# Optimization experiments

Measured on AMD Instinct MI355X. Metric: run time of the kernel, lower is better.

## Reference

```python
import jax, jax.numpy as jnp
import numpy as np

H = 128        # hidden_dim
NP = 512       # program nodes
NV = 50000     # voxel nodes
E = 800000     # cross edges (16 per voxel)
TAU = 1.0
SLOPE = 0.01   # LeakyReLU default negative slope


def setup_inputs() -> dict:
    key = jax.random.key(0)
    ks = jax.random.split(key, 12)
    s = 1.0 / np.sqrt(H)
    x = jax.random.normal(ks[0], (NP, H), dtype=jnp.float32)
    v = jax.random.normal(ks[1], (NV, H), dtype=jnp.float32)
    row0 = jax.random.randint(ks[2], (E,), 0, NP, dtype=jnp.int32)
    row1 = (jnp.arange(E, dtype=jnp.int32) % NV)  # every voxel gets E/NV edges
    cross_edge_index = jnp.stack([row0, row1])    # [2, E]
    W_program = jax.random.normal(ks[3], (H, H), dtype=jnp.float32) * s
    b_program = jnp.zeros((H,), dtype=jnp.float32)
    W_voxel = jax.random.normal(ks[4], (H, H), dtype=jnp.float32) * s
    b_voxel = jnp.zeros((H,), dtype=jnp.float32)
    W_m1 = jax.random.normal(ks[5], (H, H), dtype=jnp.float32) * s
    b_m1 = jnp.zeros((H,), dtype=jnp.float32)
    W_m2 = jax.random.normal(ks[6], (H, 1), dtype=jnp.float32) * s
    b_m2 = jnp.zeros((1,), dtype=jnp.float32)
    theta = jax.random.normal(ks[7], (H, 1), dtype=jnp.float32) * s  # xavier-like
    u = jax.random.uniform(ks[8], (E,), dtype=jnp.float32)
    gumbel_u = jnp.clip(u, 1e-7, 1.0 - 1e-7)  # avoid log(0)
    return {"x": x, "v": v, "cross_edge_index": cross_edge_index,
            "W_program": W_program, "b_program": b_program,
            "W_voxel": W_voxel, "b_voxel": b_voxel,
            "W_m1": W_m1, "b_m1": b_m1, "W_m2": W_m2, "b_m2": b_m2,
            "theta": theta, "gumbel_u": gumbel_u}


def reference(x, v, cross_edge_index, W_program, b_program, W_voxel, b_voxel,
              W_m1, b_m1, W_m2, b_m2, theta, gumbel_u):
    src = cross_edge_index[0]
    dst = cross_edge_index[1]
    x_sel = x[src]                      # [E, H] gather
    v_sel = v[dst]                      # [E, H] gather
    # mask = sigmoid(MLP(v)) : Linear -> LeakyReLU -> Linear(H,1)
    a = v @ W_m1 + b_m1
    a = jnp.where(a >= 0, a, SLOPE * a)
    mask = jax.nn.sigmoid(a @ W_m2 + b_m2)                  # [NV, 1]
    # attention logits: theta^T * tanh(Wp x_sel + Wv v_sel), summed over H
    t = jnp.tanh(x_sel @ W_program + b_program + v_sel @ W_voxel + b_voxel)
    e = jnp.sum(t * theta[:, 0], axis=-1)                   # [E]
    # Gumbel softmax: global softmax over all edges (dim=0 in torch on 1-D e)
    g = -jnp.log(-jnp.log(gumbel_u))
    y = jax.nn.softmax((e + g) / TAU)                       # [E]
    # per-voxel hard argmax (scatter_max), straight-through estimator
    seg_max = jax.ops.segment_max(y, dst, num_segments=NV)  # [NV]
    is_max = y == seg_max[dst]
    cand = jnp.where(is_max, jnp.arange(E), E)
    argmax = jax.ops.segment_min(cand, dst, num_segments=NV)  # [NV], first max per voxel
    y_hard_1 = jnp.zeros(E + 1, y.dtype).at[argmax].set(1.0)[:E]  # overflow slot for empty segments
    y_hard = jax.lax.stop_gradient(y_hard_1 - y) + y
    # scatter-sum of soft-attended program features back to voxels
    summed = jax.ops.segment_sum(x_sel * y[:, None], dst, num_segments=NV)  # [NV, H]
    v_out = v + mask * summed
    return (v_out, mask, y[:, None], y_hard[:, None])
```

## Files before the change

### kernel.cpp

```cpp
#include <hip/hip_runtime.h>

#define H     128
#define NP    512
#define NVOX  50000
#define NEDGE 800000
#define EPV   16
#define SLOPE 0.01f
#define GR    32
#define NBLK  1563
#define STRH  136
#define VSTR  132
#define C1    2.8853900817779268f
#define LOG2E 1.4426950408889634f
#define ABLK  3125

#define EXP2(x) __builtin_amdgcn_exp2f(x)
#define LOG2(x) __builtin_amdgcn_logf(x)
#define RCP(x)  __builtin_amdgcn_rcpf(x)

typedef _Float16 h16;
typedef __attribute__((ext_vector_type(4))) _Float16 h16x4;
typedef __attribute__((ext_vector_type(8))) _Float16 h16x8;
typedef __attribute__((ext_vector_type(4))) float    f32x4;

__global__ __launch_bounds__(256) void k_pre(const float* __restrict__ x,
                                             const float* __restrict__ Wp,
                                             const float* __restrict__ bp,
                                             const float* __restrict__ Wv,
                                             const float* __restrict__ Wm1,
                                             float* __restrict__ xpout,
                                             h16* __restrict__ WvThi,
                                             h16* __restrict__ WvTlo,
                                             h16* __restrict__ Wm1T) {
    __shared__ float part[H];
    int bid = blockIdx.x;
    int tid = threadIdx.x;
    if (bid < NP) {
        int row = bid;
        int col = tid & 127;
        int kh  = tid >> 7;
        int kbase = kh * 64;
        const float* xr = x + (size_t)row * H;
        float acc = 0.f;
#pragma unroll 8
        for (int k = 0; k < 64; ++k)
            acc = fmaf(xr[kbase + k], Wp[(size_t)(kbase + k) * H + col], acc);
        if (kh == 1) part[col] = acc;
        __syncthreads();
        if (kh == 0) xpout[(size_t)row * H + col] = (acc + part[col] + bp[col]) * C1;
    } else {
        int idx = (bid - NP) * 256 + tid;
        if (idx < 16384) {
            int k = idx >> 7, n = idx & 127;
            float w = Wv[idx];
            h16 hi = (h16)w;
            WvThi[n * H + k] = hi;
            WvTlo[n * H + k] = (h16)(w - (float)hi);
        } else {
            int j = idx - 16384;
            int k = j >> 7, n = j & 127;
            Wm1T[n * H + k] = (h16)Wm1[j];
        }
    }
}

__global__ __launch_bounds__(256, 4) void k_mainX(
    const float* __restrict__ v,   const float* __restrict__ x,
    const float* __restrict__ bv,  const float* __restrict__ bm1,
    const float* __restrict__ Wm2, const float* __restrict__ bm2,
    const h16* __restrict__ WvThi, const h16* __restrict__ WvTlo,
    const h16* __restrict__ Wm1T,
    const float* __restrict__ xp,  const int* __restrict__ cei,
    const float* __restrict__ theta, const float* __restrict__ gum,
    float* __restrict__ mask_out, float* __restrict__ pout,
    float* __restrict__ sump,     float* __restrict__ partial)
{
    __shared__ __align__(16) char ldsbuf[2 * GR * STRH * 2];
    h16*   vh = (h16*)ldsbuf;
    h16*   vl = vh + GR * STRH;
    float* vt = (float*)ldsbuf;
    __shared__ float ptile[EPV * GR];
    __shared__ int   ceit[EPV * GR];
    __shared__ float gumt[EPV * GR];
    __shared__ int   amtile[GR];
    __shared__ float pmbuf[4][GR];
    __shared__ float psums[4];

    int tid  = threadIdx.x;
    int base = blockIdx.x * GR;

#pragma unroll
    for (int i = 0; i < 4; ++i) {
        int f  = i * 256 + tid;
        int r  = f >> 5, c4 = f & 31;
        int gr = base + r; if (gr >= NVOX) gr = NVOX - 1;
        float4 val = *(const float4*)&v[(size_t)gr * H + c4 * 4];
        h16x4 hi, lo;
        hi.x = (h16)val.x; lo.x = (h16)(val.x - (float)hi.x);
        hi.y = (h16)val.y; lo.y = (h16)(val.y - (float)hi.y);
        hi.z = (h16)val.z; lo.z = (h16)(val.z - (float)hi.z);
        hi.w = (h16)val.w; lo.w = (h16)(val.w - (float)hi.w);
        *(h16x4*)&vh[r * STRH + c4 * 4] = hi;
        *(h16x4*)&vl[r * STRH + c4 * 4] = lo;
    }
#pragma unroll
    for (int it = 0; it < 2; ++it) {
        int idx = it * 256 + tid;
        int t = idx >> 5, c = idx & 31;
        int vx = base + c; if (vx >= NVOX) vx = NVOX - 1;
        int e = vx + t * NVOX;
        ceit[idx] = cei[e];
        gumt[idx] = gum[e];
    }
    __syncthreads();

    int wave = tid >> 6, lane = tid & 63;
    int m16 = lane & 15, quad = lane >> 4;
    int cb = wave * 32;

    f32x4 aV[2][2], aM[2][2];
#pragma unroll
    for (int rt = 0; rt < 2; ++rt)
#pragma unroll
        for (int ct = 0; ct < 2; ++ct) { aV[rt][ct] = (f32x4)0.f; aM[rt][ct] = (f32x4)0.f; }

#pragma unroll
    for (int kc = 0; kc < 4; ++kc) {
        int kofs = kc * 32 + quad * 8;
        h16x8 ah[2], al[2];
#pragma unroll
        for (int rt = 0; rt < 2; ++rt) {
            int row = rt * 16 + m16;
            ah[rt] = *(const h16x8*)&vh[row * STRH + kofs];
            al[rt] = *(const h16x8*)&vl[row * STRH + kofs];
        }
#pragma unroll
        for (int ct = 0; ct < 2; ++ct) {
            int n = cb + ct * 16 + m16;
            h16x8 bh = *(const h16x8*)&WvThi[n * H + kofs];
            h16x8 bl = *(const h16x8*)&WvTlo[n * H + kofs];
            h16x8 bm = *(const h16x8*)&Wm1T[n * H + kofs];
#pragma unroll
            for (int rt = 0; rt < 2; ++rt) {
                aV[rt][ct] = __builtin_amdgcn_mfma_f32_16x16x32_f16(ah[rt], bh, aV[rt][ct], 0, 0, 0);
                aV[rt][ct] = __builtin_amdgcn_mfma_f32_16x16x32_f16(al[rt], bh, aV[rt][ct], 0, 0, 0);
                aV[rt][ct] = __builtin_amdgcn_mfma_f32_16x16x32_f16(ah[rt], bl, aV[rt][ct], 0, 0, 0);
                aM[rt][ct] = __builtin_amdgcn_mfma_f32_16x16x32_f16(ah[rt], bm, aM[rt][ct], 0, 0, 0);
            }
        }
    }
    __syncthreads();

    float pml[2][4];
#pragma unroll
    for (int rt = 0; rt < 2; ++rt)
#pragma unroll
        for (int reg = 0; reg < 4; ++reg) pml[rt][reg] = 0.f;
#pragma unroll
    for (int ct = 0; ct < 2; ++ct) {
        int col = cb + ct * 16 + m16;
        float bvc = bv[col], bmc = bm1[col], w2c = Wm2[col];
#pragma unroll
        for (int rt = 0; rt < 2; ++rt)
#pragma unroll
            for (int reg = 0; reg < 4; ++reg) {
                int row = rt * 16 + quad * 4 + reg;
                vt[row * VSTR + col] = (aV[rt][ct][reg] + bvc) * C1;
                float m = aM[rt][ct][reg] + bmc;
                m = (m >= 0.f) ? m : SLOPE * m;
                pml[rt][reg] = fmaf(m, w2c, pml[rt][reg]);
            }
    }
#pragma unroll
    for (int off = 8; off >= 1; off >>= 1)
#pragma unroll
        for (int rt = 0; rt < 2; ++rt)
#pragma unroll
            for (int reg = 0; reg < 4; ++reg)
                pml[rt][reg] += __shfl_xor(pml[rt][reg], off, 64);
    if (m16 == 0) {
#pragma unroll
        for (int rt = 0; rt < 2; ++rt)
#pragma unroll
            for (int reg = 0; reg < 4; ++reg)
                pmbuf[wave][rt * 16 + quad * 4 + reg] = pml[rt][reg];
    }
    __syncthreads();
    if (wave == 0 && lane < GR) {
        int gr = base + lane;
        if (gr < NVOX) {
            float s = pmbuf[0][lane] + pmbuf[1][lane] + pmbuf[2][lane]
                    + pmbuf[3][lane] + bm2[0];
            mask_out[gr] = RCP(1.f + EXP2(-s * LOG2E));
        }
    }

    int g = tid >> 3, lk = tid & 7;
    int vox = base + g;
    bool valid = vox < NVOX;
    float th2[16], thsum = 0.f;
#pragma unroll
    for (int i = 0; i < 4; ++i) {
        float4 t4 = *(const float4*)&theta[(lk + 8 * i) * 4];
        th2[i * 4 + 0] = -2.f * LOG2E * t4.x; th2[i * 4 + 1] = -2.f * LOG2E * t4.y;
        th2[i * 4 + 2] = -2.f * LOG2E * t4.z; th2[i * 4 + 3] = -2.f * LOG2E * t4.w;
        thsum += LOG2E * (t4.x + t4.y + t4.z + t4.w);
    }
    const float* vr = &vt[g * VSTR];
    float4 b0 = *(const float4*)&vr[(lk +  0) * 4];
    float4 b1 = *(const float4*)&vr[(lk +  8) * 4];
    float4 b2 = *(const float4*)&vr[(lk + 16) * 4];
    float4 b3 = *(const float4*)&vr[(lk + 24) * 4];

    float4 s0 = make_float4(0.f,0.f,0.f,0.f), s1 = s0, s2 = s0, s3 = s0;
    float psum = 0.f, pmax = -1.f;
    int   pidx = 0;

    int srcC = ceit[g];
    const float4* xr0 = (const float4*)(xp + (size_t)srcC * H);
    float4 a0 = xr0[lk], a1 = xr0[lk + 8], a2 = xr0[lk + 16], a3 = xr0[lk + 24];

    for (int t = 0; t < EPV; ++t) {
        float4 n0, n1, n2, n3;
        int srcN;
        if (t < EPV - 1) {
            srcN = ceit[(t + 1) * GR + g];
            const float4* xrN = (const float4*)(xp + (size_t)srcN * H);
            n0 = xrN[lk]; n1 = xrN[lk + 8]; n2 = xrN[lk + 16]; n3 = xrN[lk + 24];
        } else {
            srcN = srcC; n0 = a0; n1 = a1; n2 = a2; n3 = a3;
        }
        const float4* xo = (const float4*)(x + (size_t)srcC * H);
        float4 c0 = xo[lk], c1 = xo[lk + 8], c2 = xo[lk + 16], c3 = xo[lk + 24];
        float wvt = -LOG2E * RCP(LOG2(gumt[t * GR + g]));

        float acc0 = thsum, acc1 = 0.f;
        acc0 = fmaf(th2[ 0], RCP(EXP2(a0.x + b0.x) + 1.f), acc0);
        acc1 = fmaf(th2[ 1], RCP(EXP2(a0.y + b0.y) + 1.f), acc1);
        acc0 = fmaf(th2[ 2], RCP(EXP2(a0.z + b0.z) + 1.f), acc0);
        acc1 = fmaf(th2[ 3], RCP(EXP2(a0.w + b0.w) + 1.f), acc1);
        acc0 = fmaf(th2[ 4], RCP(EXP2(a1.x + b1.x) + 1.f), acc0);
        acc1 = fmaf(th2[ 5], RCP(EXP2(a1.y + b1.y) + 1.f), acc1);
        acc0 = fmaf(th2[ 6], RCP(EXP2(a1.z + b1.z) + 1.f), acc0);
        acc1 = fmaf(th2[ 7], RCP(EXP2(a1.w + b1.w) + 1.f), acc1);
        acc0 = fmaf(th2[ 8], RCP(EXP2(a2.x + b2.x) + 1.f), acc0);
        acc1 = fmaf(th2[ 9], RCP(EXP2(a2.y + b2.y) + 1.f), acc1);
        acc0 = fmaf(th2[10], RCP(EXP2(a2.z + b2.z) + 1.f), acc0);
        acc1 = fmaf(th2[11], RCP(EXP2(a2.w + b2.w) + 1.f), acc1);
        acc0 = fmaf(th2[12], RCP(EXP2(a3.x + b3.x) + 1.f), acc0);
        acc1 = fmaf(th2[13], RCP(EXP2(a3.y + b3.y) + 1.f), acc1);
        acc0 = fmaf(th2[14], RCP(EXP2(a3.z + b3.z) + 1.f), acc0);
        acc1 = fmaf(th2[15], RCP(EXP2(a3.w + b3.w) + 1.f), acc1);
        float acc = acc0 + acc1;
        acc += __shfl_xor(acc, 4, 64);
        acc += __shfl_xor(acc, 2, 64);
        acc += __shfl_xor(acc, 1, 64);
        float p = EXP2(acc) * wvt;
        if (p > pmax) { pmax = p; pidx = t; }
        if (valid) psum += p;
        if (lk == 0) ptile[t * GR + g] = p;
        s0.x = fmaf(p, c0.x, s0.x); s0.y = fmaf(p, c0.y, s0.y);
        s0.z = fmaf(p, c0.z, s0.z); s0.w = fmaf(p, c0.w, s0.w);
        s1.x = fmaf(p, c1.x, s1.x); s1.y = fmaf(p, c1.y, s1.y);
        s1.z = fmaf(p, c1.z, s1.z); s1.w = fmaf(p, c1.w, s1.w);
        s2.x = fmaf(p, c2.x, s2.x); s2.y = fmaf(p, c2.y, s2.y);
        s2.z = fmaf(p, c2.z, s2.z); s2.w = fmaf(p, c2.w, s2.w);
        s3.x = fmaf(p, c3.x, s3.x); s3.y = fmaf(p, c3.y, s3.y);
        s3.z = fmaf(p, c3.z, s3.z); s3.w = fmaf(p, c3.w, s3.w);
        a0 = n0; a1 = n1; a2 = n2; a3 = n3; srcC = srcN;
    }
    if (lk == 0) amtile[g] = pidx;
    if (valid) {
        float* sr = sump + (size_t)vox * H;
        *(float4*)&sr[(lk +  0) * 4] = s0;
        *(float4*)&sr[(lk +  8) * 4] = s1;
        *(float4*)&sr[(lk + 16) * 4] = s2;
        *(float4*)&sr[(lk + 24) * 4] = s3;
    }
    psum += __shfl_xor(psum, 8, 64);
    psum += __shfl_xor(psum, 16, 64);
    psum += __shfl_xor(psum, 32, 64);
    if (lane == 0) psums[wave] = psum;
    __syncthreads();
#pragma unroll
    for (int it = 0; it < 2; ++it) {
        int idx = it * 256 + tid;
        int t = idx >> 5, c = idx & 31;
        int vox2 = base + c;
        if (vox2 < NVOX) {
            float val = ptile[t * GR + c];
            pout[vox2 + t * NVOX] = (t == amtile[c]) ? -val : val;
        }
    }
    if (tid == 0)
        partial[blockIdx.x] = psums[0] + psums[1] + psums[2] + psums[3];
}

__global__ __launch_bounds__(256) void k_out(const float* __restrict__ v,
                                             const float* __restrict__ maskp,
                                             const float* __restrict__ partial,
                                             float* __restrict__ vout,
                                             float* __restrict__ ybuf,
                                             float* __restrict__ yhard) {
    __shared__ float wsum[4];
    int tid = threadIdx.x;
    float s = 0.f;
    for (int i = tid; i < NBLK; i += 256) s += partial[i];
#pragma unroll
    for (int off = 32; off >= 1; off >>= 1) s += __shfl_xor(s, off, 64);
    if ((tid & 63) == 0) wsum[tid >> 6] = s;
    __syncthreads();
    float invS = RCP(wsum[0] + wsum[1] + wsum[2] + wsum[3]);

    int bid = blockIdx.x;
    if (bid < ABLK) {
#pragma unroll
        for (int r = 0; r < 2; ++r) {
            int i = (bid + r * ABLK) * 256 + tid;
            float4 sp = ((const float4*)vout)[i];
            float4 vv = ((const float4*)v)[i];
            float  m  = maskp[i >> 5] * invS;
            float4 o;
            o.x = fmaf(m, sp.x, vv.x); o.y = fmaf(m, sp.y, vv.y);
            o.z = fmaf(m, sp.z, vv.z); o.w = fmaf(m, sp.w, vv.w);
            ((float4*)vout)[i] = o;
        }
    } else {
        int e = (bid - ABLK) * 256 + tid;
        float pv = ybuf[e];
        ybuf[e]  = fabsf(pv) * invS;
        yhard[e] = (pv < 0.f) ? 1.f : 0.f;
    }
}

extern "C" void kernel_launch(void* const* d_in, const int* in_sizes, int n_in,
                              void* d_out, int out_size, void* d_ws, size_t ws_size,
                              hipStream_t stream) {
    (void)in_sizes; (void)n_in; (void)out_size; (void)ws_size;
    const float* x   = (const float*)d_in[0];
    const float* v   = (const float*)d_in[1];
    const int*   cei = (const int*)d_in[2];
    const float* Wp  = (const float*)d_in[3];
    const float* bp  = (const float*)d_in[4];
    const float* Wv  = (const float*)d_in[5];
    const float* bv  = (const float*)d_in[6];
    const float* Wm1 = (const float*)d_in[7];
    const float* bm1 = (const float*)d_in[8];
    const float* Wm2 = (const float*)d_in[9];
    const float* bm2 = (const float*)d_in[10];
    const float* th  = (const float*)d_in[11];
    const float* gum = (const float*)d_in[12];

    float* out   = (float*)d_out;
    float* vout  = out;
    float* maskp = out + (size_t)NVOX * H;
    float* ybuf  = maskp + NVOX;
    float* yhard = ybuf + NEDGE;
    float* xp    = yhard;
    h16*   WvThi = (h16*)(yhard + 65536);
    h16*   WvTlo = WvThi + 16384;
    h16*   Wm1T  = WvThi + 32768;
    float* partial = (float*)d_ws;

    k_pre<<<NP + 128, 256, 0, stream>>>(x, Wp, bp, Wv, Wm1, xp, WvThi, WvTlo, Wm1T);
    k_mainX<<<NBLK, 256, 0, stream>>>(v, x, bv, bm1, Wm2, bm2, WvThi, WvTlo, Wm1T,
                                      xp, cei, th, gum, maskp, ybuf, vout, partial);
    k_out<<<2 * ABLK, 256, 0, stream>>>(v, maskp, partial, vout, ybuf, yhard);
}
```

Baseline: 180.8 us.

## Halve voxel group per block, use 16 lanes per voxel and DPP reductions

Each block now handles 16 voxels instead of 32, so twice as many blocks launch, and the launch bound allows 8 blocks per CU for higher occupancy. Each voxel is processed by 16 lanes holding 8 hidden elements each instead of 8 lanes holding 16, and the shuffle reductions become DPP adds. The Gumbel log transform moves into the staging load, the LDS staging of p is dropped in favour of direct strided stores to pout, and the argmax entry is rewritten with a negated value afterwards. Bounds checks are removed because 50000 divides evenly by 16, and the direct pout writes are less coalesced than the previous tiled store.

```diff
diff --git a/kernel.cpp b/kernel.cpp
--- a/kernel.cpp
+++ b/kernel.cpp
@@ -6,8 +6,8 @@
 #define NEDGE 800000
 #define EPV   16
 #define SLOPE 0.01f
-#define GR    32
-#define NBLK  1563
+#define GR    16
+#define NBLK  3125
 #define STRH  136
 #define VSTR  132
 #define C1    2.8853900817779268f
@@ -22,6 +22,14 @@
 typedef __attribute__((ext_vector_type(4))) _Float16 h16x4;
 typedef __attribute__((ext_vector_type(8))) _Float16 h16x8;
 typedef __attribute__((ext_vector_type(4))) float    f32x4;
+
+template <int CTRL>
+__device__ __forceinline__ float dpp_add(float x) {
+    union { float f; int i; } u, r;
+    u.f = x;
+    r.i = __builtin_amdgcn_update_dpp(0, u.i, CTRL, 0xf, 0xf, true);
+    return x + r.f;
+}
 
 __global__ __launch_bounds__(256) void k_pre(const float* __restrict__ x,
                                              const float* __restrict__ Wp,
@@ -64,7 +72,7 @@
     }
 }
 
-__global__ __launch_bounds__(256, 4) void k_mainX(
+__global__ __launch_bounds__(256, 8) void k_mainX(
     const float* __restrict__ v,   const float* __restrict__ x,
     const float* __restrict__ bv,  const float* __restrict__ bm1,
     const float* __restrict__ Wm2, const float* __restrict__ bm2,
@@ -79,10 +87,8 @@
     h16*   vh = (h16*)ldsbuf;
     h16*   vl = vh + GR * STRH;
     float* vt = (float*)ldsbuf;
-    __shared__ float ptile[EPV * GR];
     __shared__ int   ceit[EPV * GR];
     __shared__ float gumt[EPV * GR];
-    __shared__ int   amtile[GR];
     __shared__ float pmbuf[4][GR];
     __shared__ float psums[4];
 
@@ -90,11 +96,10 @@
     int base = blockIdx.x * GR;
 
 #pragma unroll
-    for (int i = 0; i < 4; ++i) {
+    for (int i = 0; i < 2; ++i) {
         int f  = i * 256 + tid;
         int r  = f >> 5, c4 = f & 31;
-        int gr = base + r; if (gr >= NVOX) gr = NVOX - 1;
-        float4 val = *(const float4*)&v[(size_t)gr * H + c4 * 4];
+        float4 val = *(const float4*)&v[(size_t)(base + r) * H + c4 * 4];
         h16x4 hi, lo;
         hi.x = (h16)val.x; lo.x = (h16)(val.x - (float)hi.x);
         hi.y = (h16)val.y; lo.y = (h16)(val.y - (float)hi.y);
@@ -103,14 +108,11 @@
         *(h16x4*)&vh[r * STRH + c4 * 4] = hi;
         *(h16x4*)&vl[r * STRH + c4 * 4] = lo;
     }
-#pragma unroll
-    for (int it = 0; it < 2; ++it) {
-        int idx = it * 256 + tid;
-        int t = idx >> 5, c = idx & 31;
-        int vx = base + c; if (vx >= NVOX) vx = NVOX - 1;
-        int e = vx + t * NVOX;
-        ceit[idx] = cei[e];
-        gumt[idx] = gum[e];
+    {
+        int t = tid >> 4, c = tid & 15;
+        int e = base + c + t * NVOX;
+        ceit[tid] = cei[e];
+        gumt[tid] = -LOG2E * RCP(LOG2(gum[e]));
     }
     __syncthreads();
 
@@ -118,180 +120,132 @@
     int m16 = lane & 15, quad = lane >> 4;
     int cb = wave * 32;
 
-    f32x4 aV[2][2], aM[2][2];
-#pragma unroll
-    for (int rt = 0; rt < 2; ++rt)
-#pragma unroll
-        for (int ct = 0; ct < 2; ++ct) { aV[rt][ct] = (f32x4)0.f; aM[rt][ct] = (f32x4)0.f; }
+    f32x4 aV[2], aM[2];
+    aV[0] = (f32x4)0.f; aV[1] = (f32x4)0.f;
+    aM[0] = (f32x4)0.f; aM[1] = (f32x4)0.f;
 
 #pragma unroll
     for (int kc = 0; kc < 4; ++kc) {
         int kofs = kc * 32 + quad * 8;
-        h16x8 ah[2], al[2];
-#pragma unroll
-        for (int rt = 0; rt < 2; ++rt) {
-            int row = rt * 16 + m16;
-            ah[rt] = *(const h16x8*)&vh[row * STRH + kofs];
-            al[rt] = *(const h16x8*)&vl[row * STRH + kofs];
-        }
+        h16x8 ah = *(const h16x8*)&vh[m16 * STRH + kofs];
+        h16x8 al = *(const h16x8*)&vl[m16 * STRH + kofs];
 #pragma unroll
         for (int ct = 0; ct < 2; ++ct) {
             int n = cb + ct * 16 + m16;
             h16x8 bh = *(const h16x8*)&WvThi[n * H + kofs];
             h16x8 bl = *(const h16x8*)&WvTlo[n * H + kofs];
             h16x8 bm = *(const h16x8*)&Wm1T[n * H + kofs];
-#pragma unroll
-            for (int rt = 0; rt < 2; ++rt) {
-                aV[rt][ct] = __builtin_amdgcn_mfma_f32_16x16x32_f16(ah[rt], bh, aV[rt][ct], 0, 0, 0);
-                aV[rt][ct] = __builtin_amdgcn_mfma_f32_16x16x32_f16(al[rt], bh, aV[rt][ct], 0, 0, 0);
-                aV[rt][ct] = __builtin_amdgcn_mfma_f32_16x16x32_f16(ah[rt], bl, aV[rt][ct], 0, 0, 0);
-                aM[rt][ct] = __builtin_amdgcn_mfma_f32_16x16x32_f16(ah[rt], bm, aM[rt][ct], 0, 0, 0);
-            }
-        }
-    }
-    __syncthreads();
-
-    float pml[2][4];
-#pragma unroll
-    for (int rt = 0; rt < 2; ++rt)
-#pragma unroll
-        for (int reg = 0; reg < 4; ++reg) pml[rt][reg] = 0.f;
+            aV[ct] = __builtin_amdgcn_mfma_f32_16x16x32_f16(ah, bh, aV[ct], 0, 0, 0);
+            aV[ct] = __builtin_amdgcn_mfma_f32_16x16x32_f16(al, bh, aV[ct], 0, 0, 0);
+            aV[ct] = __builtin_amdgcn_mfma_f32_16x16x32_f16(ah, bl, aV[ct], 0, 0, 0);
+            aM[ct] = __builtin_amdgcn_mfma_f32_16x16x32_f16(ah, bm, aM[ct], 0, 0, 0);
+        }
+    }
+    __syncthreads();
+
+    float pml[4] = {0.f, 0.f, 0.f, 0.f};
 #pragma unroll
     for (int ct = 0; ct < 2; ++ct) {
         int col = cb + ct * 16 + m16;
         float bvc = bv[col], bmc = bm1[col], w2c = Wm2[col];
 #pragma unroll
-        for (int rt = 0; rt < 2; ++rt)
-#pragma unroll
-            for (int reg = 0; reg < 4; ++reg) {
-                int row = rt * 16 + quad * 4 + reg;
-                vt[row * VSTR + col] = (aV[rt][ct][reg] + bvc) * C1;
-                float m = aM[rt][ct][reg] + bmc;
-                m = (m >= 0.f) ? m : SLOPE * m;
-                pml[rt][reg] = fmaf(m, w2c, pml[rt][reg]);
-            }
-    }
-#pragma unroll
-    for (int off = 8; off >= 1; off >>= 1)
-#pragma unroll
-        for (int rt = 0; rt < 2; ++rt)
-#pragma unroll
-            for (int reg = 0; reg < 4; ++reg)
-                pml[rt][reg] += __shfl_xor(pml[rt][reg], off, 64);
+        for (int reg = 0; reg < 4; ++reg) {
+            int row = quad * 4 + reg;
+            vt[row * VSTR + col] = (aV[ct][reg] + bvc) * C1;
+            float m = aM[ct][reg] + bmc;
+            m = (m >= 0.f) ? m : SLOPE * m;
+            pml[reg] = fmaf(m, w2c, pml[reg]);
+        }
+    }
+#pragma unroll
+    for (int reg = 0; reg < 4; ++reg) {
+        pml[reg] = dpp_add<0xB1>(pml[reg]);
+        pml[reg] = dpp_add<0x4E>(pml[reg]);
+        pml[reg] = dpp_add<0x141>(pml[reg]);
+        pml[reg] = dpp_add<0x140>(pml[reg]);
+    }
     if (m16 == 0) {
 #pragma unroll
-        for (int rt = 0; rt < 2; ++rt)
-#pragma unroll
-            for (int reg = 0; reg < 4; ++reg)
-                pmbuf[wave][rt * 16 + quad * 4 + reg] = pml[rt][reg];
-    }
-    __syncthreads();
-    if (wave == 0 && lane < GR) {
-        int gr = base + lane;
-        if (gr < NVOX) {
-            float s = pmbuf[0][lane] + pmbuf[1][lane] + pmbuf[2][lane]
-                    + pmbuf[3][lane] + bm2[0];
-            mask_out[gr] = RCP(1.f + EXP2(-s * LOG2E));
-        }
-    }
-
-    int g = tid >> 3, lk = tid & 7;
+        for (int reg = 0; reg < 4; ++reg)
+            pmbuf[wave][quad * 4 + reg] = pml[reg];
+    }
+    __syncthreads();
+    if (tid < GR) {
+        float s = pmbuf[0][tid] + pmbuf[1][tid] + pmbuf[2][tid] + pmbuf[3][tid]
+                + bm2[0];
+        mask_out[base + tid] = RCP(1.f + EXP2(-s * LOG2E));
+    }
+
+    int g = tid >> 4, lk = tid & 15;
     int vox = base + g;
-    bool valid = vox < NVOX;
-    float th2[16], thsum = 0.f;
-#pragma unroll
-    for (int i = 0; i < 4; ++i) {
-        float4 t4 = *(const float4*)&theta[(lk + 8 * i) * 4];
-        th2[i * 4 + 0] = -2.f * LOG2E * t4.x; th2[i * 4 + 1] = -2.f * LOG2E * t4.y;
-        th2[i * 4 + 2] = -2.f * LOG2E * t4.z; th2[i * 4 + 3] = -2.f * LOG2E * t4.w;
-        thsum += LOG2E * (t4.x + t4.y + t4.z + t4.w);
+    float th2[8], thsum;
+    {
+        float4 ta = *(const float4*)&theta[lk * 4];
+        float4 tb = *(const float4*)&theta[(lk + 16) * 4];
+        th2[0] = -2.f * LOG2E * ta.x; th2[1] = -2.f * LOG2E * ta.y;
+        th2[2] = -2.f * LOG2E * ta.z; th2[3] = -2.f * LOG2E * ta.w;
+        th2[4] = -2.f * LOG2E * tb.x; th2[5] = -2.f * LOG2E * tb.y;
+        th2[6] = -2.f * LOG2E * tb.z; th2[7] = -2.f * LOG2E * tb.w;
+        thsum = LOG2E * (ta.x + ta.y + ta.z + ta.w + tb.x + tb.y + tb.z + tb.w);
     }
     const float* vr = &vt[g * VSTR];
-    float4 b0 = *(const float4*)&vr[(lk +  0) * 4];
-    float4 b1 = *(const float4*)&vr[(lk +  8) * 4];
-    float4 b2 = *(const float4*)&vr[(lk + 16) * 4];
-    float4 b3 = *(const float4*)&vr[(lk + 24) * 4];
-
-    float4 s0 = make_float4(0.f,0.f,0.f,0.f), s1 = s0, s2 = s0, s3 = s0;
+    float4 b0 = *(const float4*)&vr[lk * 4];
+    float4 b1 = *(const float4*)&vr[(lk + 16) * 4];
+
+    float4 s0 = make_float4(0.f, 0.f, 0.f, 0.f), s1 = s0;
     float psum = 0.f, pmax = -1.f;
     int   pidx = 0;
 
     int srcC = ceit[g];
     const float4* xr0 = (const float4*)(xp + (size_t)srcC * H);
-    float4 a0 = xr0[lk], a1 = xr0[lk + 8], a2 = xr0[lk + 16], a3 = xr0[lk + 24];
+    float4 a0 = xr0[lk], a1 = xr0[lk + 16];
 
     for (int t = 0; t < EPV; ++t) {
-        float4 n0, n1, n2, n3;
+        float4 n0, n1;
         int srcN;
         if (t < EPV - 1) {
             srcN = ceit[(t + 1) * GR + g];
             const float4* xrN = (const float4*)(xp + (size_t)srcN * H);
-            n0 = xrN[lk]; n1 = xrN[lk + 8]; n2 = xrN[lk + 16]; n3 = xrN[lk + 24];
+            n0 = xrN[lk]; n1 = xrN[lk + 16];
         } else {
-            srcN = srcC; n0 = a0; n1 = a1; n2 = a2; n3 = a3;
+            srcN = srcC; n0 = a0; n1 = a1;
         }
         const float4* xo = (const float4*)(x + (size_t)srcC * H);
-        float4 c0 = xo[lk], c1 = xo[lk + 8], c2 = xo[lk + 16], c3 = xo[lk + 24];
-        float wvt = -LOG2E * RCP(LOG2(gumt[t * GR + g]));
+        float4 c0 = xo[lk], c1 = xo[lk + 16];
+        float wvt = gumt[t * GR + g];
 
         float acc0 = thsum, acc1 = 0.f;
-        acc0 = fmaf(th2[ 0], RCP(EXP2(a0.x + b0.x) + 1.f), acc0);
-        acc1 = fmaf(th2[ 1], RCP(EXP2(a0.y + b0.y) + 1.f), acc1);
-        acc0 = fmaf(th2[ 2], RCP(EXP2(a0.z + b0.z) + 1.f), acc0);
-        acc1 = fmaf(th2[ 3], RCP(EXP2(a0.w + b0.w) + 1.f), acc1);
-        acc0 = fmaf(th2[ 4], RCP(EXP2(a1.x + b1.x) + 1.f), acc0);
-        acc1 = fmaf(th2[ 5], RCP(EXP2(a1.y + b1.y) + 1.f), acc1);
-        acc0 = fmaf(th2[ 6], RCP(EXP2(a1.z + b1.z) + 1.f), acc0);
-        acc1 = fmaf(th2[ 7], RCP(EXP2(a1.w + b1.w) + 1.f), acc1);
-        acc0 = fmaf(th2[ 8], RCP(EXP2(a2.x + b2.x) + 1.f), acc0);
-        acc1 = fmaf(th2[ 9], RCP(EXP2(a2.y + b2.y) + 1.f), acc1);
-        acc0 = fmaf(th2[10], RCP(EXP2(a2.z + b2.z) + 1.f), acc0);
-        acc1 = fmaf(th2[11], RCP(EXP2(a2.w + b2.w) + 1.f), acc1);
-        acc0 = fmaf(th2[12], RCP(EXP2(a3.x + b3.x) + 1.f), acc0);
-        acc1 = fmaf(th2[13], RCP(EXP2(a3.y + b3.y) + 1.f), acc1);
-        acc0 = fmaf(th2[14], RCP(EXP2(a3.z + b3.z) + 1.f), acc0);
-        acc1 = fmaf(th2[15], RCP(EXP2(a3.w + b3.w) + 1.f), acc1);
+        acc0 = fmaf(th2[0], RCP(EXP2(a0.x + b0.x) + 1.f), acc0);
+        acc1 = fmaf(th2[1], RCP(EXP2(a0.y + b0.y) + 1.f), acc1);
+        acc0 = fmaf(th2[2], RCP(EXP2(a0.z + b0.z) + 1.f), acc0);
+        acc1 = fmaf(th2[3], RCP(EXP2(a0.w + b0.w) + 1.f), acc1);
+        acc0 = fmaf(th2[4], RCP(EXP2(a1.x + b1.x) + 1.f), acc0);
+        acc1 = fmaf(th2[5], RCP(EXP2(a1.y + b1.y) + 1.f), acc1);
+        acc0 = fmaf(th2[6], RCP(EXP2(a1.z + b1.z) + 1.f), acc0);
+        acc1 = fmaf(th2[7], RCP(EXP2(a1.w + b1.w) + 1.f), acc1);
         float acc = acc0 + acc1;
-        acc += __shfl_xor(acc, 4, 64);
-        acc += __shfl_xor(acc, 2, 64);
-        acc += __shfl_xor(acc, 1, 64);
+        acc = dpp_add<0xB1>(acc);
+        acc = dpp_add<0x4E>(acc);
+        acc = dpp_add<0x141>(acc);
+        acc = dpp_add<0x140>(acc);
         float p = EXP2(acc) * wvt;
         if (p > pmax) { pmax = p; pidx = t; }
-        if (valid) psum += p;
-        if (lk == 0) ptile[t * GR + g] = p;
+        psum += p;
+        if (lk == 0) pout[vox + t * NVOX] = p;
         s0.x = fmaf(p, c0.x, s0.x); s0.y = fmaf(p, c0.y, s0.y);
         s0.z = fmaf(p, c0.z, s0.z); s0.w = fmaf(p, c0.w, s0.w);
         s1.x = fmaf(p, c1.x, s1.x); s1.y = fmaf(p, c1.y, s1.y);
         s1.z = fmaf(p, c1.z, s1.z); s1.w = fmaf(p, c1.w, s1.w);
-        s2.x = fmaf(p, c2.x, s2.x); s2.y = fmaf(p, c2.y, s2.y);
-        s2.z = fmaf(p, c2.z, s2.z); s2.w = fmaf(p, c2.w, s2.w);
-        s3.x = fmaf(p, c3.x, s3.x); s3.y = fmaf(p, c3.y, s3.y);
-        s3.z = fmaf(p, c3.z, s3.z); s3.w = fmaf(p, c3.w, s3.w);
-        a0 = n0; a1 = n1; a2 = n2; a3 = n3; srcC = srcN;
-    }
-    if (lk == 0) amtile[g] = pidx;
-    if (valid) {
-        float* sr = sump + (size_t)vox * H;
-        *(float4*)&sr[(lk +  0) * 4] = s0;
-        *(float4*)&sr[(lk +  8) * 4] = s1;
-        *(float4*)&sr[(lk + 16) * 4] = s2;
-        *(float4*)&sr[(lk + 24) * 4] = s3;
-    }
-    psum += __shfl_xor(psum, 8, 64);
+        a0 = n0; a1 = n1; srcC = srcN;
+    }
+    if (lk == 0) pout[vox + pidx * NVOX] = -pmax;
+    float* sr = sump + (size_t)vox * H;
+    *(float4*)&sr[lk * 4]        = s0;
+    *(float4*)&sr[(lk + 16) * 4] = s1;
     psum += __shfl_xor(psum, 16, 64);
     psum += __shfl_xor(psum, 32, 64);
     if (lane == 0) psums[wave] = psum;
     __syncthreads();
-#pragma unroll
-    for (int it = 0; it < 2; ++it) {
-        int idx = it * 256 + tid;
-        int t = idx >> 5, c = idx & 31;
-        int vox2 = base + c;
-        if (vox2 < NVOX) {
-            float val = ptile[t * GR + c];
-            pout[vox2 + t * NVOX] = (t == amtile[c]) ? -val : val;
-        }
-    }
     if (tid == 0)
         partial[blockIdx.x] = psums[0] + psums[1] + psums[2] + psums[3];
 }
```

Result: slower. 230.8 us (+27.6%).
